# Kernel optimization log

Measured on AMD Instinct MI355X. Metric: run time of the kernel, lower is better.

The kernel has to match this reference:

```python
import jax, jax.numpy as jnp
import numpy as np
import math

B, S, H, NH = 2, 2048, 1024, 16
DK = H // NH
EPS = 1e-5

def setup_inputs() -> dict:
    key = jax.random.key(0)
    ks = jax.random.split(key, 8)
    sd = 0.02
    return {
        "x": jax.random.normal(ks[0], (B, S, H), dtype=jnp.float32),
        "ln1_w": jnp.ones((H,), jnp.float32),
        "ln1_b": jnp.zeros((H,), jnp.float32),
        "W_qkv": jax.random.normal(ks[1], (H, 3 * H), jnp.float32) * sd,
        "b_qkv": jnp.zeros((3 * H,), jnp.float32),
        "W_o": jax.random.normal(ks[2], (H, H), jnp.float32) * sd,
        "b_o": jnp.zeros((H,), jnp.float32),
        "ln2_w": jnp.ones((H,), jnp.float32),
        "ln2_b": jnp.zeros((H,), jnp.float32),
        "W_fc": jax.random.normal(ks[3], (H, 4 * H), jnp.float32) * sd,
        "b_fc": jnp.zeros((4 * H,), jnp.float32),
        "W_proj": jax.random.normal(ks[4], (4 * H, H), jnp.float32) * sd,
        "b_proj": jnp.zeros((H,), jnp.float32),
    }

def _layernorm(x, w, b):
    mu = jnp.mean(x, axis=-1, keepdims=True)
    var = jnp.mean(jnp.square(x - mu), axis=-1, keepdims=True)
    return (x - mu) * jax.lax.rsqrt(var + EPS) * w + b

def _attn(x, W_qkv, b_qkv, W_o, b_o):
    bs, seq, _ = x.shape
    qkv = x @ W_qkv + b_qkv                      # [b,s,3H]
    q, k, v = jnp.split(qkv, 3, axis=-1)
    q = q.reshape(bs, seq, NH, DK).transpose(0, 2, 1, 3)  # [b,h,s,d]
    k = k.reshape(bs, seq, NH, DK).transpose(0, 2, 1, 3)
    v = v.reshape(bs, seq, NH, DK).transpose(0, 2, 1, 3)
    scores = jnp.einsum("bhqd,bhkd->bhqk", q, k) / math.sqrt(DK)
    causal = jnp.tril(jnp.ones((seq, seq), bool))
    scores = jnp.where(causal, scores, -jnp.inf)
    attn = jax.nn.softmax(scores, axis=-1)
    out = jnp.einsum("bhqk,bhkd->bhqd", attn, v)
    out = out.transpose(0, 2, 1, 3).reshape(bs, seq, H)
    return out @ W_o + b_o

def reference(x, ln1_w, ln1_b, W_qkv, b_qkv, W_o, b_o, ln2_w, ln2_b, W_fc, b_fc, W_proj, b_proj):
    x = x + _attn(_layernorm(x, ln1_w, ln1_b), W_qkv, b_qkv, W_o, b_o)
    h = _layernorm(x, ln2_w, ln2_b)
    h = jax.nn.gelu(h @ W_fc + b_fc, approximate=False) @ W_proj + b_proj
    return x + h
```

## Files before the change

kernel.cpp:

```cpp
#include <hip/hip_runtime.h>
#include <hip/hip_bf16.h>
#include <math.h>

#define H_DIM 1024
#define SEQ   2048
#define BATCH 2
#define NHEAD 16
#define DKV   64
#define ROWS  (BATCH*SEQ)
#define QSCALE 0.18033688f

typedef __attribute__((ext_vector_type(8))) short short8;
typedef __attribute__((ext_vector_type(4))) float f32x4;

static __device__ __forceinline__ unsigned short f32_bf16(float f) {
    unsigned int u = __builtin_bit_cast(unsigned int, f);
    u += 0x7FFF + ((u >> 16) & 1);
    return (unsigned short)(u >> 16);
}

static __device__ __forceinline__ float fast_erf(float x) {
    float ax = fabsf(x);
    float t = 1.0f / fmaf(0.3275911f, ax, 1.0f);
    float p = t * fmaf(t, fmaf(t, fmaf(t, fmaf(t, 1.061405429f, -1.453152027f),
                                       1.421413741f), -0.284496736f), 0.254829592f);
    float y = fmaf(-p, __expf(-ax * ax), 1.0f);
    return copysignf(y, x);
}

static __device__ __forceinline__ void gload16(const unsigned short* g, unsigned short* l) {
    __builtin_amdgcn_global_load_lds(
        (const __attribute__((address_space(1))) void*)g,
        (__attribute__((address_space(3))) void*)l,
        16, 0, 0);
}

__global__ __launch_bounds__(256) void transpose_bf16(const float* __restrict__ in,
                                                      unsigned short* __restrict__ out,
                                                      int K, int N) {
    __shared__ float tile[32][33];
    int n0 = blockIdx.x * 32, k0 = blockIdx.y * 32;
    int tx = threadIdx.x & 31, ty = threadIdx.x >> 5;
    #pragma unroll
    for (int i = 0; i < 4; ++i)
        tile[ty + i * 8][tx] = in[(size_t)(k0 + ty + i * 8) * N + n0 + tx];
    __syncthreads();
    #pragma unroll
    for (int i = 0; i < 4; ++i)
        out[(size_t)(n0 + ty + i * 8) * K + k0 + tx] = f32_bf16(tile[tx][ty + i * 8]);
}

__global__ __launch_bounds__(256) void ln_bf16(const float* __restrict__ x,
                                               const float* __restrict__ w,
                                               const float* __restrict__ bb,
                                               unsigned short* __restrict__ out) {
    int row = blockIdx.x;
    int tid = threadIdx.x;
    float4 v = ((const float4*)(x + (size_t)row * H_DIM))[tid];
    float s  = v.x + v.y + v.z + v.w;
    float s2 = v.x*v.x + v.y*v.y + v.z*v.z + v.w*v.w;
    #pragma unroll
    for (int off = 1; off < 64; off <<= 1) {
        s  += __shfl_xor(s,  off, 64);
        s2 += __shfl_xor(s2, off, 64);
    }
    __shared__ float red[8];
    int wv = tid >> 6;
    if ((tid & 63) == 0) { red[wv] = s; red[4 + wv] = s2; }
    __syncthreads();
    s  = red[0] + red[1] + red[2] + red[3];
    s2 = red[4] + red[5] + red[6] + red[7];
    float mu = s * (1.0f / H_DIM);
    float rs = rsqrtf(s2 * (1.0f / H_DIM) - mu * mu + 1e-5f);
    float4 wv4 = ((const float4*)w)[tid];
    float4 bv4 = ((const float4*)bb)[tid];
    ushort4 o;
    o.x = f32_bf16((v.x - mu) * rs * wv4.x + bv4.x);
    o.y = f32_bf16((v.y - mu) * rs * wv4.y + bv4.y);
    o.z = f32_bf16((v.z - mu) * rs * wv4.z + bv4.z);
    o.w = f32_bf16((v.w - mu) * rs * wv4.w + bv4.w);
    ((ushort4*)(out + (size_t)row * H_DIM))[tid] = o;
}

template<int EPI>
static __device__ __forceinline__ void epi_store(f32x4 a, int row0, int col, int N,
                                                 const float* __restrict__ bias,
                                                 const float* __restrict__ resid,
                                                 float* __restrict__ outF,
                                                 unsigned short* __restrict__ outH,
                                                 unsigned short* __restrict__ outH2) {
    float bv = bias[col];
    if (EPI == 4 && col >= 2048) {
        int bb = row0 >> 11, ss = row0 & 2047;
        int hd = col - 2048;
        ushort4 u;
        u.x = f32_bf16(a[0] + bv);
        u.y = f32_bf16(a[1] + bv);
        u.z = f32_bf16(a[2] + bv);
        u.w = f32_bf16(a[3] + bv);
        *(ushort4*)&outH2[((size_t)bb * 1024 + hd) * SEQ + ss] = u;
    } else {
        #pragma unroll
        for (int j = 0; j < 4; ++j) {
            int row = row0 + j;
            size_t idx = (size_t)row * N + col;
            float c = a[j] + bv;
            if (EPI == 0) {
                outF[idx] = c;
            } else if (EPI == 1) {
                outF[idx] = resid[idx] + c;
            } else if (EPI == 2) {
                float g = 0.5f * c * (1.0f + fast_erf(c * 0.70710678118f));
                outH[idx] = f32_bf16(g);
            } else if (EPI == 3) {
                outH[idx] = f32_bf16(c);
            } else {
                float c2 = (col < 1024) ? c * QSCALE : c;
                outH[(size_t)row * 2048 + col] = f32_bf16(c2);
            }
        }
    }
}

template<int EPI, int NI>
__global__ __launch_bounds__(512) void gemmT(const unsigned short* __restrict__ A,
                                             const unsigned short* __restrict__ Bt,
                                             const float* __restrict__ bias,
                                             const float* __restrict__ resid,
                                             float* __restrict__ outF,
                                             unsigned short* __restrict__ outH,
                                             unsigned short* __restrict__ outH2,
                                             int gx, int N, int K) {
    constexpr int BN = NI * 32;
    constexpr int WN = BN / 4;
    constexpr int NT = WN / 16;
    __shared__ __attribute__((aligned(16))) unsigned short As[128][64];
    __shared__ __attribute__((aligned(16))) unsigned short Bs[BN][64];
    int tid = threadIdx.x;
    int w = tid >> 6, l = tid & 63;
    int l15 = l & 15, lg = l >> 4;
    int wm = w & 1, wn = w >> 1;

    int qq = gridDim.x >> 3;
    int wg = (blockIdx.x & 7) * qq + (blockIdx.x >> 3);
    int bm = wg / gx, bn = wg - bm * gx;
    int m0 = bm * 128, n0 = bn * BN;

    f32x4 acc[4][NT] = {};

    const unsigned short* aptr[2];
    unsigned short* lA[2];
    #pragma unroll
    for (int j = 0; j < 2; ++j) {
        int slot = j * 512 + tid;
        int row = slot >> 3;
        int lchunk = (slot & 7) ^ (row & 7);
        aptr[j] = A + (size_t)(m0 + row) * K + lchunk * 8;
        lA[j] = &As[0][0] + (size_t)slot * 8 - l * 8;
    }
    const unsigned short* bptr[NI / 2];
    unsigned short* lB[NI / 2];
    #pragma unroll
    for (int j = 0; j < NI / 2; ++j) {
        int slot = j * 512 + tid;
        int row = slot >> 3;
        int lchunk = (slot & 7) ^ (row & 7);
        bptr[j] = Bt + (size_t)(n0 + row) * K + lchunk * 8;
        lB[j] = &Bs[0][0] + (size_t)slot * 8 - l * 8;
    }
    int swz[2];
    swz[0] = ((0 + lg) ^ (l15 & 7)) * 8;
    swz[1] = ((4 + lg) ^ (l15 & 7)) * 8;
    const unsigned short* pA = &As[wm * 64 + l15][0];
    const unsigned short* pB = &Bs[wn * WN + l15][0];

    for (int k0 = 0; k0 < K; k0 += 64) {
        __syncthreads();
        #pragma unroll
        for (int j = 0; j < 2; ++j) gload16(aptr[j] + k0, lA[j]);
        #pragma unroll
        for (int j = 0; j < NI / 2; ++j) gload16(bptr[j] + k0, lB[j]);
        __syncthreads();

        #pragma unroll
        for (int ks = 0; ks < 2; ++ks) {
            short8 af[4], bf[NT];
            #pragma unroll
            for (int mi = 0; mi < 4; ++mi)
                af[mi] = *(const short8*)(pA + mi * 16 * 64 + swz[ks]);
            #pragma unroll
            for (int ni = 0; ni < NT; ++ni)
                bf[ni] = *(const short8*)(pB + ni * 16 * 64 + swz[ks]);
            #pragma unroll
            for (int mi = 0; mi < 4; ++mi)
                #pragma unroll
                for (int ni = 0; ni < NT; ++ni)
                    acc[mi][ni] = __builtin_amdgcn_mfma_f32_16x16x32_bf16(af[mi], bf[ni], acc[mi][ni], 0, 0, 0);
        }
    }

    #pragma unroll
    for (int mi = 0; mi < 4; ++mi)
        #pragma unroll
        for (int ni = 0; ni < NT; ++ni)
            epi_store<EPI>(acc[mi][ni], m0 + wm * 64 + mi * 16 + lg * 4,
                           n0 + wn * WN + ni * 16 + l15, N, bias, resid, outF, outH, outH2);
}

__global__ __launch_bounds__(512) void attn_mfma(const unsigned short* __restrict__ qk,
                                                 const unsigned short* __restrict__ vT,
                                                 unsigned short* __restrict__ out) {
    int bid = blockIdx.x;
    int swz = (bid & 7) * 64 + (bid >> 3);
    int b  = swz >> 8;
    int h  = (swz >> 4) & 15;
    int qt = 15 - (swz & 15);
    int tid = threadIdx.x;
    int w = tid >> 6, l = tid & 63;
    int l15 = l & 15, lg = l >> 4;

    __shared__ __attribute__((aligned(16))) unsigned short Ks[64][72];
    __shared__ __attribute__((aligned(16))) unsigned short Vt[64][72];
    __shared__ __attribute__((aligned(16))) unsigned short Ps[8][16][72];

    int qrow = qt * 128 + w * 16 + l15;
    short8 qf[2];
    {
        const unsigned short* qp = qk + (size_t)(b * SEQ + qrow) * 2048 + h * DKV + lg * 8;
        qf[0] = *(const short8*)qp;
        qf[1] = *(const short8*)(qp + 32);
    }
    short8 vf5;
    #pragma unroll
    for (int i = 0; i < 8; ++i) vf5[i] = (l15 == 0) ? (short)0x3F80 : (short)0;

    int srow = tid >> 3;
    int scol = (tid & 7) * 8;
    const unsigned short* kbase = qk + (size_t)(b * SEQ + srow) * 2048 + 1024 + h * DKV + scol;
    const unsigned short* vbase = vT + ((size_t)(b * NHEAD + h) * DKV + srow) * SEQ + scol;

    short8 kr = *(const short8*)kbase;
    short8 vr = *(const short8*)vbase;

    float m = -1e30f;
    f32x4 oacc[4] = {};
    f32x4 oext = {};

    int nt = 2 * qt + 2;
    for (int kt = 0; kt < nt; ++kt) {
        __syncthreads();
        *(short8*)&Ks[srow][scol] = kr;
        *(short8*)&Vt[srow][scol] = vr;
        __syncthreads();
        if (kt + 1 < nt) {
            kr = *(const short8*)(kbase + (size_t)(kt + 1) * 64 * 2048);
            vr = *(const short8*)(vbase + (kt + 1) * 64);
        }

        f32x4 sc[4] = {};
        __builtin_amdgcn_s_setprio(1);
        #pragma unroll
        for (int dstep = 0; dstep < 2; ++dstep) {
            #pragma unroll
            for (int st = 0; st < 4; ++st) {
                short8 kf = *(const short8*)&Ks[st * 16 + l15][dstep * 32 + lg * 8];
                sc[st] = __builtin_amdgcn_mfma_f32_16x16x32_bf16(kf, qf[dstep], sc[st], 0, 0, 0);
            }
        }
        __builtin_amdgcn_s_setprio(0);

        int klim = qrow - kt * 64;
        float pv[4][4];
        float pmax = -1e30f;
        #pragma unroll
        for (int st = 0; st < 4; ++st) {
            #pragma unroll
            for (int j = 0; j < 4; ++j) {
                float s = sc[st][j];
                if (st * 16 + lg * 4 + j > klim) s = -1e30f;
                pv[st][j] = s;
                pmax = fmaxf(pmax, s);
            }
        }

        if (!__all(pmax - m <= 8.0f)) {
            float pr = fmaxf(pmax, __shfl_xor(pmax, 16, 64));
            pr = fmaxf(pr, __shfl_xor(pr, 32, 64));
            float mn = fmaxf(m, pr);
            float scl = exp2f(m - mn);
            #pragma unroll
            for (int d = 0; d < 4; ++d)
                #pragma unroll
                for (int j = 0; j < 4; ++j)
                    oacc[d][j] *= scl;
            #pragma unroll
            for (int j = 0; j < 4; ++j) oext[j] *= scl;
            m = mn;
        }

        #pragma unroll
        for (int st = 0; st < 4; ++st) {
            float p0 = exp2f(pv[st][0] - m);
            float p1 = exp2f(pv[st][1] - m);
            float p2 = exp2f(pv[st][2] - m);
            float p3 = exp2f(pv[st][3] - m);
            unsigned int ua, ub;
            asm("v_cvt_pk_bf16_f32 %0, %1, %2" : "=v"(ua) : "v"(p0), "v"(p1));
            asm("v_cvt_pk_bf16_f32 %0, %1, %2" : "=v"(ub) : "v"(p2), "v"(p3));
            uint2 u = make_uint2(ua, ub);
            *(uint2*)&Ps[w][l15][st * 16 + lg * 4] = u;
        }

        __builtin_amdgcn_s_setprio(1);
        #pragma unroll
        for (int ks = 0; ks < 2; ++ks) {
            short8 pf = *(const short8*)&Ps[w][l15][ks * 32 + lg * 8];
            #pragma unroll
            for (int d = 0; d < 4; ++d) {
                short8 vf = *(const short8*)&Vt[d * 16 + l15][ks * 32 + lg * 8];
                oacc[d] = __builtin_amdgcn_mfma_f32_16x16x32_bf16(vf, pf, oacc[d], 0, 0, 0);
            }
            oext = __builtin_amdgcn_mfma_f32_16x16x32_bf16(vf5, pf, oext, 0, 0, 0);
        }
        __builtin_amdgcn_s_setprio(0);
    }

    float lsum = __shfl(oext[0], l15, 64);
    float inv = 1.0f / lsum;
    size_t ob = (size_t)(b * SEQ + qrow) * H_DIM + h * DKV;
    #pragma unroll
    for (int d = 0; d < 4; ++d) {
        ushort4 u;
        #pragma unroll
        for (int j = 0; j < 4; ++j)
            ((unsigned short*)&u)[j] = f32_bf16(oacc[d][j] * inv);
        *(ushort4*)&out[ob + d * 16 + lg * 4] = u;
    }
}

extern "C" void kernel_launch(void* const* d_in, const int* in_sizes, int n_in,
                              void* d_out, int out_size, void* d_ws, size_t ws_size,
                              hipStream_t stream) {
    const float* x     = (const float*)d_in[0];
    const float* ln1w  = (const float*)d_in[1];
    const float* ln1b  = (const float*)d_in[2];
    const float* Wqkv  = (const float*)d_in[3];
    const float* bqkv  = (const float*)d_in[4];
    const float* Wo    = (const float*)d_in[5];
    const float* bo    = (const float*)d_in[6];
    const float* ln2w  = (const float*)d_in[7];
    const float* ln2b  = (const float*)d_in[8];
    const float* Wfc   = (const float*)d_in[9];
    const float* bfc   = (const float*)d_in[10];
    const float* Wproj = (const float*)d_in[11];
    const float* bproj = (const float*)d_in[12];
    float* out = (float*)d_out;

    char* ws = (char*)d_ws;
    size_t off = 0;
    auto take = [&](size_t bytes) {
        void* p = ws + off;
        off += (bytes + 255) & ~(size_t)255;
        return p;
    };

    unsigned short* WqT  = (unsigned short*)take((size_t)3072 * 1024 * 2);
    unsigned short* WoT  = (unsigned short*)take((size_t)1024 * 1024 * 2);
    unsigned short* WfcT = (unsigned short*)take((size_t)4096 * 1024 * 2);
    unsigned short* WpT  = (unsigned short*)take((size_t)1024 * 4096 * 2);
    unsigned short* xn1   = (unsigned short*)take((size_t)ROWS * 1024 * 2);
    unsigned short* qk_h  = (unsigned short*)take((size_t)ROWS * 2048 * 2);
    unsigned short* vT    = (unsigned short*)take((size_t)ROWS * 1024 * 2);
    unsigned short* attn  = (unsigned short*)take((size_t)ROWS * 1024 * 2);
    float*          x1    = (float*)take((size_t)ROWS * 1024 * 4);
    unsigned short* xn2   = (unsigned short*)take((size_t)ROWS * 1024 * 2);
    unsigned short* hbuf  = (unsigned short*)take((size_t)ROWS * 4096 * 2);

    transpose_bf16<<<dim3(3072 / 32, 1024 / 32), 256, 0, stream>>>(Wqkv,  WqT,  1024, 3072);
    transpose_bf16<<<dim3(1024 / 32, 1024 / 32), 256, 0, stream>>>(Wo,    WoT,  1024, 1024);
    transpose_bf16<<<dim3(4096 / 32, 1024 / 32), 256, 0, stream>>>(Wfc,   WfcT, 1024, 4096);
    transpose_bf16<<<dim3(1024 / 32, 4096 / 32), 256, 0, stream>>>(Wproj, WpT,  4096, 1024);

    ln_bf16<<<ROWS, 256, 0, stream>>>(x, ln1w, ln1b, xn1);

    gemmT<4, 4><<<768, 512, 0, stream>>>(xn1, WqT, bqkv, nullptr, nullptr, qk_h, vT, 24, 3072, 1024);

    attn_mfma<<<512, 512, 0, stream>>>(qk_h, vT, attn);

    gemmT<1, 2><<<512, 512, 0, stream>>>(attn, WoT, bo, x, x1, nullptr, nullptr, 16, 1024, 1024);

    ln_bf16<<<ROWS, 256, 0, stream>>>(x1, ln2w, ln2b, xn2);

    gemmT<2, 4><<<1024, 512, 0, stream>>>(xn2, WfcT, bfc, nullptr, nullptr, hbuf, nullptr, 32, 4096, 1024);

    gemmT<1, 2><<<512, 512, 0, stream>>>(hbuf, WpT, bproj, x1, out, nullptr, nullptr, 16, 1024, 4096);
}
```

Before: 248.8 us.

## Rework attention into balanced paired passes, bf16 residual, and XCD-aware GEMM tile mapping

```diff
diff --git a/kernel.cpp b/kernel.cpp
--- a/kernel.cpp
+++ b/kernel.cpp
@@ -18,6 +18,9 @@
     u += 0x7FFF + ((u >> 16) & 1);
     return (unsigned short)(u >> 16);
 }
+static __device__ __forceinline__ float bf16_f32(unsigned short h) {
+    return __builtin_bit_cast(float, (unsigned int)h << 16);
+}
 
 static __device__ __forceinline__ float fast_erf(float x) {
     float ax = fabsf(x);
@@ -50,13 +53,20 @@
         out[(size_t)(n0 + ty + i * 8) * K + k0 + tx] = f32_bf16(tile[tx][ty + i * 8]);
 }
 
-__global__ __launch_bounds__(256) void ln_bf16(const float* __restrict__ x,
-                                               const float* __restrict__ w,
-                                               const float* __restrict__ bb,
-                                               unsigned short* __restrict__ out) {
+template<int BF16IN>
+__global__ __launch_bounds__(256) void ln_any(const void* __restrict__ xin,
+                                              const float* __restrict__ w,
+                                              const float* __restrict__ bb,
+                                              unsigned short* __restrict__ out) {
     int row = blockIdx.x;
     int tid = threadIdx.x;
-    float4 v = ((const float4*)(x + (size_t)row * H_DIM))[tid];
+    float4 v;
+    if (BF16IN) {
+        ushort4 u = ((const ushort4*)((const unsigned short*)xin + (size_t)row * H_DIM))[tid];
+        v.x = bf16_f32(u.x); v.y = bf16_f32(u.y); v.z = bf16_f32(u.z); v.w = bf16_f32(u.w);
+    } else {
+        v = ((const float4*)((const float*)xin + (size_t)row * H_DIM))[tid];
+    }
     float s  = v.x + v.y + v.z + v.w;
     float s2 = v.x*v.x + v.y*v.y + v.z*v.z + v.w*v.w;
     #pragma unroll
@@ -114,6 +124,10 @@
                 outH[idx] = f32_bf16(g);
             } else if (EPI == 3) {
                 outH[idx] = f32_bf16(c);
+            } else if (EPI == 5) {
+                outH[idx] = f32_bf16(resid[idx] + c);
+            } else if (EPI == 6) {
+                outF[idx] = bf16_f32(outH2[idx]) + c;
             } else {
                 float c2 = (col < 1024) ? c * QSCALE : c;
                 outH[(size_t)row * 2048 + col] = f32_bf16(c2);
@@ -130,7 +144,7 @@
                                              float* __restrict__ outF,
                                              unsigned short* __restrict__ outH,
                                              unsigned short* __restrict__ outH2,
-                                             int gx, int N, int K) {
+                                             int cm, int cn, int ncc, int N, int K) {
     constexpr int BN = NI * 32;
     constexpr int WN = BN / 4;
     constexpr int NT = WN / 16;
@@ -141,9 +155,11 @@
     int l15 = l & 15, lg = l >> 4;
     int wm = w & 1, wn = w >> 1;
 
-    int qq = gridDim.x >> 3;
-    int wg = (blockIdx.x & 7) * qq + (blockIdx.x >> 3);
-    int bm = wg / gx, bn = wg - bm * gx;
+    int c = blockIdx.x & 7, lwg = blockIdx.x >> 3;
+    int lm = lwg / cn, ln = lwg - lm * cn;
+    int ccr = c / ncc;
+    int bm = ccr * cm + lm;
+    int bn = (c - ccr * ncc) * cn + ln;
     int m0 = bm * 128, n0 = bn * BN;
 
     f32x4 acc[4][NT] = {};
@@ -207,135 +223,175 @@
                            n0 + wn * WN + ni * 16 + l15, N, bias, resid, outF, outH, outH2);
 }
 
-__global__ __launch_bounds__(512) void attn_mfma(const unsigned short* __restrict__ qk,
+__global__ __launch_bounds__(256) void attn_mfma(const unsigned short* __restrict__ qk,
                                                  const unsigned short* __restrict__ vT,
                                                  unsigned short* __restrict__ out) {
     int bid = blockIdx.x;
     int swz = (bid & 7) * 64 + (bid >> 3);
     int b  = swz >> 8;
     int h  = (swz >> 4) & 15;
-    int qt = 15 - (swz & 15);
+    int p  = swz & 15;
     int tid = threadIdx.x;
     int w = tid >> 6, l = tid & 63;
     int l15 = l & 15, lg = l >> 4;
 
-    __shared__ __attribute__((aligned(16))) unsigned short Ks[64][72];
-    __shared__ __attribute__((aligned(16))) unsigned short Vt[64][72];
-    __shared__ __attribute__((aligned(16))) unsigned short Ps[8][16][72];
-
-    int qrow = qt * 128 + w * 16 + l15;
-    short8 qf[2];
-    {
+    __shared__ __attribute__((aligned(16))) unsigned short Ks[2][64][64];
+    __shared__ __attribute__((aligned(16))) unsigned short Vt[2][64][64];
+    __shared__ __attribute__((aligned(16))) unsigned short Ps[4][16][72];
+
+    short8 vf5;
+    #pragma unroll
+    for (int i = 0; i < 8; ++i) vf5[i] = (l15 == 0) ? (short)0x3F80 : (short)0;
+
+    int sr = tid >> 2;
+    int c0 = (tid & 3) * 2, c1 = c0 + 1;
+    int sp0 = ((c0 ^ (sr & 7)) * 8);
+    int sp1 = ((c1 ^ (sr & 7)) * 8);
+    const unsigned short* kb0 = qk + (size_t)(b * SEQ + sr) * 2048 + 1024 + h * DKV + c0 * 8;
+    const unsigned short* kb1 = kb0 + 8;
+    const unsigned short* vb0 = vT + ((size_t)(b * NHEAD + h) * DKV + sr) * SEQ + c0 * 8;
+    const unsigned short* vb1 = vb0 + 8;
+
+    int rk0 = ((0 + lg) ^ (l15 & 7)) * 8;
+    int rk1 = ((4 + lg) ^ (l15 & 7)) * 8;
+
+    auto run_pass = [&](int qt) {
+        int qrow = qt * 64 + w * 16 + l15;
         const unsigned short* qp = qk + (size_t)(b * SEQ + qrow) * 2048 + h * DKV + lg * 8;
-        qf[0] = *(const short8*)qp;
-        qf[1] = *(const short8*)(qp + 32);
-    }
-    short8 vf5;
-    #pragma unroll
-    for (int i = 0; i < 8; ++i) vf5[i] = (l15 == 0) ? (short)0x3F80 : (short)0;
-
-    int srow = tid >> 3;
-    int scol = (tid & 7) * 8;
-    const unsigned short* kbase = qk + (size_t)(b * SEQ + srow) * 2048 + 1024 + h * DKV + scol;
-    const unsigned short* vbase = vT + ((size_t)(b * NHEAD + h) * DKV + srow) * SEQ + scol;
-
-    short8 kr = *(const short8*)kbase;
-    short8 vr = *(const short8*)vbase;
-
-    float m = -1e30f;
-    f32x4 oacc[4] = {};
-    f32x4 oext = {};
-
-    int nt = 2 * qt + 2;
-    for (int kt = 0; kt < nt; ++kt) {
+        short8 qf0 = *(const short8*)qp;
+        short8 qf1 = *(const short8*)(qp + 32);
+        float m = -1e30f;
+        f32x4 oacc[4] = {};
+        f32x4 oext = {};
+        int nt = qt + 1;
+
+        short8 kr0 = *(const short8*)kb0;
+        short8 kr1 = *(const short8*)kb1;
+        short8 vr0 = *(const short8*)vb0;
+        short8 vr1 = *(const short8*)vb1;
+        *(short8*)&Ks[0][sr][sp0] = kr0;
+        *(short8*)&Ks[0][sr][sp1] = kr1;
+        *(short8*)&Vt[0][sr][sp0] = vr0;
+        *(short8*)&Vt[0][sr][sp1] = vr1;
+        if (nt > 1) {
+            kr0 = *(const short8*)(kb0 + (size_t)64 * 2048);
+            kr1 = *(const short8*)(kb1 + (size_t)64 * 2048);
+            vr0 = *(const short8*)(vb0 + 64);
+            vr1 = *(const short8*)(vb1 + 64);
+        }
         __syncthreads();
-        *(short8*)&Ks[srow][scol] = kr;
-        *(short8*)&Vt[srow][scol] = vr;
-        __syncthreads();
-        if (kt + 1 < nt) {
-            kr = *(const short8*)(kbase + (size_t)(kt + 1) * 64 * 2048);
-            vr = *(const short8*)(vbase + (kt + 1) * 64);
+
+        for (int t = 0; t < nt; ++t) {
+            int nb = (t + 1) & 1;
+            if (t + 1 < nt) {
+                *(short8*)&Ks[nb][sr][sp0] = kr0;
+                *(short8*)&Ks[nb][sr][sp1] = kr1;
+                *(short8*)&Vt[nb][sr][sp0] = vr0;
+                *(short8*)&Vt[nb][sr][sp1] = vr1;
+                if (t + 2 < nt) {
+                    kr0 = *(const short8*)(kb0 + (size_t)(t + 2) * 64 * 2048);
+                    kr1 = *(const short8*)(kb1 + (size_t)(t + 2) * 64 * 2048);
+                    vr0 = *(const short8*)(vb0 + (t + 2) * 64);
+                    vr1 = *(const short8*)(vb1 + (t + 2) * 64);
+                }
+            }
+            int bu = t & 1;
+
+            f32x4 sc[4] = {};
+            __builtin_amdgcn_s_setprio(1);
+            #pragma unroll
+            for (int st = 0; st < 4; ++st) {
+                short8 kf0 = *(const short8*)&Ks[bu][st * 16 + l15][rk0];
+                sc[st] = __builtin_amdgcn_mfma_f32_16x16x32_bf16(kf0, qf0, sc[st], 0, 0, 0);
+                short8 kf1 = *(const short8*)&Ks[bu][st * 16 + l15][rk1];
+                sc[st] = __builtin_amdgcn_mfma_f32_16x16x32_bf16(kf1, qf1, sc[st], 0, 0, 0);
+            }
+            __builtin_amdgcn_s_setprio(0);
+
+            float pv[4][4];
+            float pmax = -1e30f;
+            if (t == qt) {
+                int klim = qrow - t * 64;
+                #pragma unroll
+                for (int st = 0; st < 4; ++st) {
+                    #pragma unroll
+                    for (int j = 0; j < 4; ++j) {
+                        float s = sc[st][j];
+                        if (st * 16 + lg * 4 + j > klim) s = -1e30f;
+                        pv[st][j] = s;
+                        pmax = fmaxf(pmax, s);
+                    }
+                }
+            } else {
+                #pragma unroll
+                for (int st = 0; st < 4; ++st) {
+                    #pragma unroll
+                    for (int j = 0; j < 4; ++j) {
+                        pv[st][j] = sc[st][j];
+                        pmax = fmaxf(pmax, sc[st][j]);
+                    }
+                }
+            }
+
+            if (!__all(pmax - m <= 8.0f)) {
+                float pr = fmaxf(pmax, __shfl_xor(pmax, 16, 64));
+                pr = fmaxf(pr, __shfl_xor(pr, 32, 64));
+                float mn = fmaxf(m, pr);
+                float scl2 = exp2f(m - mn);
+                #pragma unroll
+                for (int d = 0; d < 4; ++d)
+                    #pragma unroll
+                    for (int j = 0; j < 4; ++j)
+                        oacc[d][j] *= scl2;
+                #pragma unroll
+                for (int j = 0; j < 4; ++j) oext[j] *= scl2;
+                m = mn;
+            }
+
+            #pragma unroll
+            for (int st = 0; st < 4; ++st) {
+                float p0 = exp2f(pv[st][0] - m);
+                float p1 = exp2f(pv[st][1] - m);
+                float p2 = exp2f(pv[st][2] - m);
+                float p3 = exp2f(pv[st][3] - m);
+                unsigned int ua, ub;
+                asm("v_cvt_pk_bf16_f32 %0, %1, %2" : "=v"(ua) : "v"(p0), "v"(p1));
+                asm("v_cvt_pk_bf16_f32 %0, %1, %2" : "=v"(ub) : "v"(p2), "v"(p3));
+                uint2 u = make_uint2(ua, ub);
+                *(uint2*)&Ps[w][l15][st * 16 + lg * 4] = u;
+            }
+
+            __builtin_amdgcn_s_setprio(1);
+            #pragma unroll
+            for (int ks = 0; ks < 2; ++ks) {
+                short8 pf = *(const short8*)&Ps[w][l15][ks * 32 + lg * 8];
+                int rv = (ks == 0) ? rk0 : rk1;
+                #pragma unroll
+                for (int d = 0; d < 4; ++d) {
+                    short8 vf = *(const short8*)&Vt[bu][d * 16 + l15][rv];
+                    oacc[d] = __builtin_amdgcn_mfma_f32_16x16x32_bf16(vf, pf, oacc[d], 0, 0, 0);
+                }
+                oext = __builtin_amdgcn_mfma_f32_16x16x32_bf16(vf5, pf, oext, 0, 0, 0);
+            }
+            __builtin_amdgcn_s_setprio(0);
+            __syncthreads();
         }
 
-        f32x4 sc[4] = {};
-        __builtin_amdgcn_s_setprio(1);
-        #pragma unroll
-        for (int dstep = 0; dstep < 2; ++dstep) {
-            #pragma unroll
-            for (int st = 0; st < 4; ++st) {
-                short8 kf = *(const short8*)&Ks[st * 16 + l15][dstep * 32 + lg * 8];
-                sc[st] = __builtin_amdgcn_mfma_f32_16x16x32_bf16(kf, qf[dstep], sc[st], 0, 0, 0);
-            }
+        float lsum = __shfl(oext[0], l15, 64);
+        float inv = 1.0f / lsum;
+        size_t ob = (size_t)(b * SEQ + qrow) * H_DIM + h * DKV;
+        #pragma unroll
+        for (int d = 0; d < 4; ++d) {
+            ushort4 u;
+            #pragma unroll
+            for (int j = 0; j < 4; ++j)
+                ((unsigned short*)&u)[j] = f32_bf16(oacc[d][j] * inv);
+            *(ushort4*)&out[ob + d * 16 + lg * 4] = u;
         }
-        __builtin_amdgcn_s_setprio(0);
-
-        int klim = qrow - kt * 64;
-        float pv[4][4];
-        float pmax = -1e30f;
-        #pragma unroll
-        for (int st = 0; st < 4; ++st) {
-            #pragma unroll
-            for (int j = 0; j < 4; ++j) {
-                float s = sc[st][j];
-                if (st * 16 + lg * 4 + j > klim) s = -1e30f;
-                pv[st][j] = s;
-                pmax = fmaxf(pmax, s);
-            }
-        }
-
-        if (!__all(pmax - m <= 8.0f)) {
-            float pr = fmaxf(pmax, __shfl_xor(pmax, 16, 64));
-            pr = fmaxf(pr, __shfl_xor(pr, 32, 64));
-            float mn = fmaxf(m, pr);
-            float scl = exp2f(m - mn);
-            #pragma unroll
-            for (int d = 0; d < 4; ++d)
-                #pragma unroll
-                for (int j = 0; j < 4; ++j)
-                    oacc[d][j] *= scl;
-            #pragma unroll
-            for (int j = 0; j < 4; ++j) oext[j] *= scl;
-            m = mn;
-        }
-
-        #pragma unroll
-        for (int st = 0; st < 4; ++st) {
-            float p0 = exp2f(pv[st][0] - m);
-            float p1 = exp2f(pv[st][1] - m);
-            float p2 = exp2f(pv[st][2] - m);
-            float p3 = exp2f(pv[st][3] - m);
-            unsigned int ua, ub;
-            asm("v_cvt_pk_bf16_f32 %0, %1, %2" : "=v"(ua) : "v"(p0), "v"(p1));
-            asm("v_cvt_pk_bf16_f32 %0, %1, %2" : "=v"(ub) : "v"(p2), "v"(p3));
-            uint2 u = make_uint2(ua, ub);
-            *(uint2*)&Ps[w][l15][st * 16 + lg * 4] = u;
-        }
-
-        __builtin_amdgcn_s_setprio(1);
-        #pragma unroll
-        for (int ks = 0; ks < 2; ++ks) {
-            short8 pf = *(const short8*)&Ps[w][l15][ks * 32 + lg * 8];
-            #pragma unroll
-            for (int d = 0; d < 4; ++d) {
-                short8 vf = *(const short8*)&Vt[d * 16 + l15][ks * 32 + lg * 8];
-                oacc[d] = __builtin_amdgcn_mfma_f32_16x16x32_bf16(vf, pf, oacc[d], 0, 0, 0);
-            }
-            oext = __builtin_amdgcn_mfma_f32_16x16x32_bf16(vf5, pf, oext, 0, 0, 0);
-        }
-        __builtin_amdgcn_s_setprio(0);
-    }
-
-    float lsum = __shfl(oext[0], l15, 64);
-    float inv = 1.0f / lsum;
-    size_t ob = (size_t)(b * SEQ + qrow) * H_DIM + h * DKV;
-    #pragma unroll
-    for (int d = 0; d < 4; ++d) {
-        ushort4 u;
-        #pragma unroll
-        for (int j = 0; j < 4; ++j)
-            ((unsigned short*)&u)[j] = f32_bf16(oacc[d][j] * inv);
-        *(ushort4*)&out[ob + d * 16 + lg * 4] = u;
-    }
+    };
+
+    run_pass(31 - p);
+    run_pass(p);
 }
 
 extern "C" void kernel_launch(void* const* d_in, const int* in_sizes, int n_in,
@@ -372,7 +428,7 @@
     unsigned short* qk_h  = (unsigned short*)take((size_t)ROWS * 2048 * 2);
     unsigned short* vT    = (unsigned short*)take((size_t)ROWS * 1024 * 2);
     unsigned short* attn  = (unsigned short*)take((size_t)ROWS * 1024 * 2);
-    float*          x1    = (float*)take((size_t)ROWS * 1024 * 4);
+    unsigned short* x1h   = (unsigned short*)take((size_t)ROWS * 1024 * 2);
     unsigned short* xn2   = (unsigned short*)take((size_t)ROWS * 1024 * 2);
     unsigned short* hbuf  = (unsigned short*)take((size_t)ROWS * 4096 * 2);
 
@@ -381,17 +437,17 @@
     transpose_bf16<<<dim3(4096 / 32, 1024 / 32), 256, 0, stream>>>(Wfc,   WfcT, 1024, 4096);
     transpose_bf16<<<dim3(1024 / 32, 4096 / 32), 256, 0, stream>>>(Wproj, WpT,  4096, 1024);
 
-    ln_bf16<<<ROWS, 256, 0, stream>>>(x, ln1w, ln1b, xn1);
-
-    gemmT<4, 4><<<768, 512, 0, stream>>>(xn1, WqT, bqkv, nullptr, nullptr, qk_h, vT, 24, 3072, 1024);
-
-    attn_mfma<<<512, 512, 0, stream>>>(qk_h, vT, attn);
-
-    gemmT<1, 2><<<512, 512, 0, stream>>>(attn, WoT, bo, x, x1, nullptr, nullptr, 16, 1024, 1024);
-
-    ln_bf16<<<ROWS, 256, 0, stream>>>(x1, ln2w, ln2b, xn2);
-
-    gemmT<2, 4><<<1024, 512, 0, stream>>>(xn2, WfcT, bfc, nullptr, nullptr, hbuf, nullptr, 32, 4096, 1024);
-
-    gemmT<1, 2><<<512, 512, 0, stream>>>(hbuf, WpT, bproj, x1, out, nullptr, nullptr, 16, 1024, 4096);
-}
+    ln_any<0><<<ROWS, 256, 0, stream>>>(x, ln1w, ln1b, xn1);
+
+    gemmT<4, 4><<<768, 512, 0, stream>>>(xn1, WqT, bqkv, nullptr, nullptr, qk_h, vT, 8, 12, 2, 3072, 1024);
+
+    attn_mfma<<<512, 256, 0, stream>>>(qk_h, vT, attn);
+
+    gemmT<5, 2><<<512, 512, 0, stream>>>(attn, WoT, bo, x, nullptr, x1h, nullptr, 4, 16, 1, 1024, 1024);
+
+    ln_any<1><<<ROWS, 256, 0, stream>>>(x1h, ln2w, ln2b, xn2);
+
+    gemmT<2, 4><<<1024, 512, 0, stream>>>(xn2, WfcT, bfc, nullptr, nullptr, hbuf, nullptr, 8, 16, 2, 4096, 1024);
+
+    gemmT<6, 2><<<512, 512, 0, stream>>>(hbuf, WpT, bproj, nullptr, out, nullptr, x1h, 4, 16, 1, 1024, 4096);
+}
```

Measured after the change: 220.8 us. 11.2% less time.
